# Kernel optimization log

Measured on AMD Instinct MI355X. Metric: run time of the kernel, lower is better.

The kernel has to match this reference:

```python
import jax, jax.numpy as jnp
import numpy as np

G = 128  # voxel grid extent per axis (positions are integer voxel coords in [0, G))
K = 3    # kernel size per axis -> 27 offsets


def setup_inputs() -> dict:
    key = jax.random.key(0)
    k1, k2, k3 = jax.random.split(key, 3)
    N, Cin, Cout = 500000, 32, 32
    features = jax.random.normal(k1, (N, Cin), dtype=jnp.float32)
    in_positions = jax.random.randint(k2, (N, 3), 0, G, dtype=jnp.int32)
    # learned conv weight: one [Cin, Cout] matrix per kernel offset (27 total)
    weight = jax.random.normal(k3, (K ** 3, Cin, Cout), dtype=jnp.float32) * 0.05
    return {"features": features, "in_positions": in_positions, "weight": weight}


def _hash(pos):
    # unique linear key for integer voxel coords in [0, G)^3
    return (pos[:, 0] * G + pos[:, 1]) * G + pos[:, 2]


def reference(features, in_positions, weight):
    # Submanifold sparse conv (kernel 3x3x3, odd -> offset 0, out_positions == in_positions,
    # voxel_size = 1.0, no bias, no normalize):
    # for each active voxel, gather active neighbors at each of the 27 kernel offsets,
    # transform with the per-offset weight matrix, and accumulate.
    N = features.shape[0]
    # dense hash table: voxel key -> row index in features, -1 if inactive
    table = jnp.full((G * G * G,), -1, dtype=jnp.int32)
    table = table.at[_hash(in_positions)].set(jnp.arange(N, dtype=jnp.int32))

    out = jnp.zeros((N, weight.shape[-1]), dtype=features.dtype)
    r = K // 2
    k = 0
    for dx in range(-r, r + 1):
        for dy in range(-r, r + 1):
            for dz in range(-r, r + 1):
                npos = in_positions + jnp.array([dx, dy, dz], dtype=jnp.int32)
                inside = jnp.all((npos >= 0) & (npos < G), axis=1)
                idx = table[jnp.where(inside, _hash(npos), 0)]
                valid = inside & (idx >= 0)
                # gather active neighbor features; zero where neighbor inactive
                gathered = jnp.where(valid[:, None], features[jnp.maximum(idx, 0)], 0.0)
                out = out + gathered @ weight[k]  # [N, Cout]
                k += 1
    return out
```

## Files before the change

kernel.cpp:

```cpp
#include <hip/hip_runtime.h>


#define GRID 128
#define CIN 32
#define COUT 32
#define NOFF 27

typedef __attribute__((ext_vector_type(8))) short bf16x8;
typedef __attribute__((ext_vector_type(4))) float f32x4;

__device__ inline unsigned short f2bf(float x) {
    union { float f; unsigned u; } v; v.f = x;
    unsigned r = v.u + 0x7fff + ((v.u >> 16) & 1);
    return (unsigned short)(r >> 16);
}

__global__ void prep_kernel(const float* __restrict__ feats,
                            const int* __restrict__ pos,
                            const float* __restrict__ wt,
                            int* __restrict__ table,
                            unsigned* __restrict__ featsB,
                            unsigned short* __restrict__ wtT,
                            int N, int elems4) {
    int i = blockIdx.x * 256 + threadIdx.x;
    if (i < elems4) {
        float4 v = *(const float4*)(feats + 4 * (size_t)i);
        unsigned lo = (unsigned)f2bf(v.x) | ((unsigned)f2bf(v.y) << 16);
        unsigned hi = (unsigned)f2bf(v.z) | ((unsigned)f2bf(v.w) << 16);
        uint2 o; o.x = lo; o.y = hi;
        *(uint2*)(featsB + 2 * (size_t)i) = o;
    }
    if (i < N) {
        int x = pos[3 * i], y = pos[3 * i + 1], z = pos[3 * i + 2];
        atomicMax(&table[(x * GRID + y) * GRID + z], i);
    }
    if (i < NOFF * CIN * COUT) {
        int k = i >> 10, r = i & 1023, ci = r >> 5, co = r & 31;
        wtT[k * 1024 + co * 32 + ci] = f2bf(wt[i]);
    }
}

__global__ __launch_bounds__(1024, 8)
void conv_kernel(const unsigned short* __restrict__ featsB,
                 const int* __restrict__ pos,
                 const unsigned short* __restrict__ wtT,
                 const int* __restrict__ table,
                 float* __restrict__ out, int N) {
    __shared__ __align__(16) unsigned short ldsw[NOFF * 1024];

    int tid = threadIdx.x;
    int wave = tid >> 6, lane = tid & 63;
    int m = lane & 15, quad = lane >> 4;
    int tile = blockIdx.x * 16 + wave;
    int base = tile * 16;
    int g = base + m;
    bool gv = g < N;

    int x = 0, y = 0, z = 0;
    if (gv) { x = pos[3 * g]; y = pos[3 * g + 1]; z = pos[3 * g + 2]; }
    int h = (x * GRID + y) * GRID + z;
    bool v0[3] = {gv && x > 0, gv, gv && x < GRID - 1};
    bool v1[3] = {gv && y > 0, gv, gv && y < GRID - 1};
    bool v2[3] = {gv && z > 0, gv, gv && z < GRID - 1};

    int ids[NOFF];
#pragma unroll
    for (int k = 0; k < NOFF; ++k) {
        const int dx = k / 9, dy = (k / 3) % 3, dz = k % 3;
        bool ok = v0[dx] && v1[dy] && v2[dz];
        int hk = h + (dx - 1) * GRID * GRID + (dy - 1) * GRID + (dz - 1);
        hk = ok ? hk : 0;
        int id = table[hk];
        ids[k] = ok ? id : -1;
    }

    {
        const uint4* src = (const uint4*)wtT;
        uint4* dst = (uint4*)ldsw;
        for (int e = tid; e < NOFF * 1024 * 2 / 16; e += 1024)
            dst[e] = src[e];
    }
    __syncthreads();

    f32x4 acc0 = {0.f, 0.f, 0.f, 0.f};
    f32x4 acc1 = {0.f, 0.f, 0.f, 0.f};
    const unsigned short* wb = ldsw + m * 32 + quad * 8;

#pragma unroll
    for (int k = 0; k < NOFF; ++k) {
        int id = ids[k];
        int row = (id >= 0 ? id : 0) * CIN;
        bf16x8 a = *(const bf16x8*)(featsB + row + quad * 8);
        if (id < 0) a = (bf16x8){0, 0, 0, 0, 0, 0, 0, 0};

        bf16x8 b0 = *(const bf16x8*)(wb + k * 1024);
        bf16x8 b1 = *(const bf16x8*)(wb + k * 1024 + 512);

        acc0 = __builtin_amdgcn_mfma_f32_16x16x32_bf16(a, b0, acc0, 0, 0, 0);
        acc1 = __builtin_amdgcn_mfma_f32_16x16x32_bf16(a, b1, acc1, 0, 0, 0);
    }

#pragma unroll
    for (int i = 0; i < 4; ++i) {
        int p = base + quad * 4 + i;
        if (p < N) {
            out[(size_t)p * COUT + m]      = acc0[i];
            out[(size_t)p * COUT + m + 16] = acc1[i];
        }
    }
}

extern "C" void kernel_launch(void* const* d_in, const int* in_sizes, int n_in,
                              void* d_out, int out_size, void* d_ws, size_t ws_size,
                              hipStream_t stream) {
    const float* feats = (const float*)d_in[0];
    const int*   pos   = (const int*)d_in[1];
    const float* wt    = (const float*)d_in[2];
    float* out = (float*)d_out;
    int N = in_sizes[0] / CIN;

    char* ws = (char*)d_ws;
    int* table = (int*)ws;
    size_t table_bytes = (size_t)GRID * GRID * GRID * sizeof(int);
    unsigned short* wtT = (unsigned short*)(ws + table_bytes);
    unsigned short* featsB = (unsigned short*)(ws + table_bytes + 65536);

    hipMemsetAsync(table, 0xFF, table_bytes, stream);

    int elems4 = N * CIN / 4;
    prep_kernel<<<(elems4 + 255) / 256, 256, 0, stream>>>(
        feats, pos, wt, table, (unsigned*)featsB, wtT, N, elems4);

    int numTiles = (N + 15) / 16;
    int blocks = (numTiles + 15) / 16;
    conv_kernel<<<blocks, 1024, 0, stream>>>(featsB, pos, wtT, table, out, N);
}
```

Baseline: 254.7 us.

## Sort voxels by Morton bucket to localize neighbor gathers, remap XCD blocks

Adds a counting sort of voxels into 32768 Morton-ordered 4x4x4 buckets (histogram, single-block scan, scatter). The hash table and bf16 features are rewritten in sorted order, and outputs are scattered back through origId. The aim is spatial locality, so neighbor feature gathers hit L2 cache. Block IDs are also remapped so contiguous tiles land on the same XCD, and weights are held in registers instead of being reread from LDS. In exchange it adds several kernels, a serial single-block scan, atomics and an indirect output scatter.

```diff
diff --git a/kernel.cpp b/kernel.cpp
--- a/kernel.cpp
+++ b/kernel.cpp
@@ -5,6 +5,7 @@
 #define CIN 32
 #define COUT 32
 #define NOFF 27
+#define NBUCKET 32768
 
 typedef __attribute__((ext_vector_type(8))) short bf16x8;
 typedef __attribute__((ext_vector_type(4))) float f32x4;
@@ -15,24 +16,29 @@
     return (unsigned short)(r >> 16);
 }
 
-__global__ void prep_kernel(const float* __restrict__ feats,
-                            const int* __restrict__ pos,
+__device__ inline unsigned spread3(unsigned v) {
+    v &= 31u;
+    v = (v | (v << 16)) & 0x030000FFu;
+    v = (v | (v << 8))  & 0x0300F00Fu;
+    v = (v | (v << 4))  & 0x030C30C3u;
+    v = (v | (v << 2))  & 0x09249249u;
+    return v;
+}
+__device__ inline int morton_bucket(int x, int y, int z) {
+    return (int)(spread3(x >> 2) | (spread3(y >> 2) << 1) | (spread3(z >> 2) << 2));
+}
+
+__global__ void hist_kernel(const int* __restrict__ pos,
                             const float* __restrict__ wt,
                             int* __restrict__ table,
-                            unsigned* __restrict__ featsB,
-                            unsigned short* __restrict__ wtT,
-                            int N, int elems4) {
+                            int* __restrict__ hist,
+                            unsigned short* __restrict__ wtT, int N) {
     int i = blockIdx.x * 256 + threadIdx.x;
-    if (i < elems4) {
-        float4 v = *(const float4*)(feats + 4 * (size_t)i);
-        unsigned lo = (unsigned)f2bf(v.x) | ((unsigned)f2bf(v.y) << 16);
-        unsigned hi = (unsigned)f2bf(v.z) | ((unsigned)f2bf(v.w) << 16);
-        uint2 o; o.x = lo; o.y = hi;
-        *(uint2*)(featsB + 2 * (size_t)i) = o;
-    }
     if (i < N) {
         int x = pos[3 * i], y = pos[3 * i + 1], z = pos[3 * i + 2];
-        atomicMax(&table[(x * GRID + y) * GRID + z], i);
+        int h = (x * GRID + y) * GRID + z;
+        atomicMax(&table[h], i);
+        atomicAdd(&hist[morton_bucket(x, y, z)], 1);
     }
     if (i < NOFF * CIN * COUT) {
         int k = i >> 10, r = i & 1023, ci = r >> 5, co = r & 31;
@@ -40,25 +46,86 @@
     }
 }
 
+__global__ __launch_bounds__(1024) void scan_kernel(int* __restrict__ hist) {
+    __shared__ int sums[1024];
+    int t = threadIdx.x;
+    int base = t * 32;
+    int v[32];
+#pragma unroll
+    for (int j = 0; j < 32; ++j) v[j] = hist[base + j];
+    int s = 0;
+#pragma unroll
+    for (int j = 0; j < 32; ++j) { int tmp = v[j]; v[j] = s; s += tmp; }
+    sums[t] = s;
+    __syncthreads();
+    for (int off = 1; off < 1024; off <<= 1) {
+        int add = (t >= off) ? sums[t - off] : 0;
+        __syncthreads();
+        sums[t] += add;
+        __syncthreads();
+    }
+    int excl = sums[t] - s;
+#pragma unroll
+    for (int j = 0; j < 32; ++j) hist[base + j] = excl + v[j];
+}
+
+__global__ void scatter_kernel(const int* __restrict__ pos,
+                               int* __restrict__ hist,
+                               int* __restrict__ table,
+                               int* __restrict__ keyS,
+                               int* __restrict__ origId, int N) {
+    int i = blockIdx.x * 256 + threadIdx.x;
+    if (i >= N) return;
+    int x = pos[3 * i], y = pos[3 * i + 1], z = pos[3 * i + 2];
+    int h = (x * GRID + y) * GRID + z;
+    int slot = atomicAdd(&hist[morton_bucket(x, y, z)], 1);
+    keyS[slot] = h;
+    origId[slot] = i;
+    if (table[h] == i) table[h] = -(slot + 2);
+}
+
+__global__ void convert_kernel(const float* __restrict__ feats,
+                               const int* __restrict__ origId,
+                               uint4* __restrict__ featsB, int N4) {
+    int j = blockIdx.x * 256 + threadIdx.x;
+    if (j >= N4) return;
+    int slot = j >> 2, t = j & 3;
+    int o = origId[slot];
+    const float4* s = (const float4*)(feats + (size_t)o * CIN + t * 8);
+    float4 a = s[0], b = s[1];
+    uint4 r;
+    r.x = (unsigned)f2bf(a.x) | ((unsigned)f2bf(a.y) << 16);
+    r.y = (unsigned)f2bf(a.z) | ((unsigned)f2bf(a.w) << 16);
+    r.z = (unsigned)f2bf(b.x) | ((unsigned)f2bf(b.y) << 16);
+    r.w = (unsigned)f2bf(b.z) | ((unsigned)f2bf(b.w) << 16);
+    featsB[j] = r;
+}
+
 __global__ __launch_bounds__(1024, 8)
 void conv_kernel(const unsigned short* __restrict__ featsB,
-                 const int* __restrict__ pos,
+                 const int* __restrict__ keyS,
                  const unsigned short* __restrict__ wtT,
                  const int* __restrict__ table,
+                 const int* __restrict__ origId,
                  float* __restrict__ out, int N) {
     __shared__ __align__(16) unsigned short ldsw[NOFF * 1024];
+
+    int nwg = (int)gridDim.x;
+    int orig = (int)blockIdx.x;
+    int q8 = nwg >> 3, r8 = nwg & 7;
+    int xcd = orig & 7, lin = orig >> 3;
+    int bid = (xcd < r8 ? xcd * (q8 + 1) : r8 * (q8 + 1) + (xcd - r8) * q8) + lin;
 
     int tid = threadIdx.x;
     int wave = tid >> 6, lane = tid & 63;
     int m = lane & 15, quad = lane >> 4;
-    int tile = blockIdx.x * 16 + wave;
+    int tile = bid * 16 + wave;
     int base = tile * 16;
     int g = base + m;
     bool gv = g < N;
 
-    int x = 0, y = 0, z = 0;
-    if (gv) { x = pos[3 * g]; y = pos[3 * g + 1]; z = pos[3 * g + 2]; }
-    int h = (x * GRID + y) * GRID + z;
+    int key = gv ? keyS[g] : 0;
+    int x = key >> 14, y = (key >> 7) & 127, z = key & 127;
     bool v0[3] = {gv && x > 0, gv, gv && x < GRID - 1};
     bool v1[3] = {gv && y > 0, gv, gv && y < GRID - 1};
     bool v2[3] = {gv && z > 0, gv, gv && z < GRID - 1};
@@ -68,7 +135,7 @@
     for (int k = 0; k < NOFF; ++k) {
         const int dx = k / 9, dy = (k / 3) % 3, dz = k % 3;
         bool ok = v0[dx] && v1[dy] && v2[dz];
-        int hk = h + (dx - 1) * GRID * GRID + (dy - 1) * GRID + (dz - 1);
+        int hk = key + (dx - 1) * GRID * GRID + (dy - 1) * GRID + (dz - 1);
         hk = ok ? hk : 0;
         int id = table[hk];
         ids[k] = ok ? id : -1;
@@ -77,35 +144,39 @@
     {
         const uint4* src = (const uint4*)wtT;
         uint4* dst = (uint4*)ldsw;
-        for (int e = tid; e < NOFF * 1024 * 2 / 16; e += 1024)
-            dst[e] = src[e];
+        for (int e = tid; e < NOFF * 1024 * 2 / 16; e += 1024) dst[e] = src[e];
     }
     __syncthreads();
+
+    bf16x8 w0[NOFF], w1[NOFF];
+    const unsigned short* wb = ldsw + m * 32 + quad * 8;
+#pragma unroll
+    for (int k = 0; k < NOFF; ++k) {
+        w0[k] = *(const bf16x8*)(wb + k * 1024);
+        w1[k] = *(const bf16x8*)(wb + k * 1024 + 512);
+    }
 
     f32x4 acc0 = {0.f, 0.f, 0.f, 0.f};
     f32x4 acc1 = {0.f, 0.f, 0.f, 0.f};
-    const unsigned short* wb = ldsw + m * 32 + quad * 8;
 
 #pragma unroll
     for (int k = 0; k < NOFF; ++k) {
         int id = ids[k];
-        int row = (id >= 0 ? id : 0) * CIN;
+        bool val = id < -1;
+        int row = val ? (-id - 2) * CIN : 0;
         bf16x8 a = *(const bf16x8*)(featsB + row + quad * 8);
-        if (id < 0) a = (bf16x8){0, 0, 0, 0, 0, 0, 0, 0};
-
-        bf16x8 b0 = *(const bf16x8*)(wb + k * 1024);
-        bf16x8 b1 = *(const bf16x8*)(wb + k * 1024 + 512);
-
-        acc0 = __builtin_amdgcn_mfma_f32_16x16x32_bf16(a, b0, acc0, 0, 0, 0);
-        acc1 = __builtin_amdgcn_mfma_f32_16x16x32_bf16(a, b1, acc1, 0, 0, 0);
+        if (!val) a = (bf16x8){0, 0, 0, 0, 0, 0, 0, 0};
+        acc0 = __builtin_amdgcn_mfma_f32_16x16x32_bf16(a, w0[k], acc0, 0, 0, 0);
+        acc1 = __builtin_amdgcn_mfma_f32_16x16x32_bf16(a, w1[k], acc1, 0, 0, 0);
     }
 
 #pragma unroll
     for (int i = 0; i < 4; ++i) {
         int p = base + quad * 4 + i;
         if (p < N) {
-            out[(size_t)p * COUT + m]      = acc0[i];
-            out[(size_t)p * COUT + m + 16] = acc1[i];
+            int o = origId[p];
+            out[(size_t)o * COUT + m]      = acc0[i];
+            out[(size_t)o * COUT + m + 16] = acc1[i];
         }
     }
 }
@@ -120,18 +191,25 @@
     int N = in_sizes[0] / CIN;
 
     char* ws = (char*)d_ws;
-    int* table = (int*)ws;
-    size_t table_bytes = (size_t)GRID * GRID * GRID * sizeof(int);
-    unsigned short* wtT = (unsigned short*)(ws + table_bytes);
-    unsigned short* featsB = (unsigned short*)(ws + table_bytes + 65536);
-
-    hipMemsetAsync(table, 0xFF, table_bytes, stream);
-
-    int elems4 = N * CIN / 4;
-    prep_kernel<<<(elems4 + 255) / 256, 256, 0, stream>>>(
-        feats, pos, wt, table, (unsigned*)featsB, wtT, N, elems4);
+    size_t off = 0;
+    int* table = (int*)(ws + off);            off += (size_t)GRID * GRID * GRID * 4;
+    unsigned short* wtT = (unsigned short*)(ws + off); off += 65536;
+    int* hist = (int*)(ws + off);             off += NBUCKET * 4;
+    int* keyS = (int*)(ws + off);             off += 2097152;
+    int* origId = (int*)(ws + off);           off += 2097152;
+    unsigned short* featsB = (unsigned short*)(ws + off);
+
+    hipMemsetAsync(table, 0xFF, (size_t)GRID * GRID * GRID * 4, stream);
+    hipMemsetAsync(hist, 0, NBUCKET * 4, stream);
+
+    int blocksN = (N + 255) / 256;
+    hist_kernel<<<blocksN, 256, 0, stream>>>(pos, wt, table, hist, wtT, N);
+    scan_kernel<<<1, 1024, 0, stream>>>(hist);
+    scatter_kernel<<<blocksN, 256, 0, stream>>>(pos, hist, table, keyS, origId, N);
+    convert_kernel<<<(N * 4 + 255) / 256, 256, 0, stream>>>(feats, origId,
+                                                            (uint4*)featsB, N * 4);
 
     int numTiles = (N + 15) / 16;
-    int blocks = (numTiles + 15) / 16;
-    conv_kernel<<<blocks, 1024, 0, stream>>>(featsB, pos, wtT, table, out, N);
-}
+    int nwg = (numTiles + 15) / 16;
+    conv_kernel<<<nwg, 1024, 0, stream>>>(featsB, keyS, wtT, table, origId, out, N);
+}
```

Result: slower. 314.5 us (+23.5%).

## Software-pipeline neighbor gathers with inline asm loads and a zero sentinel row

Applied to the files above, without the earlier changes.

Adds a zero row at the front of the bf16 feature buffer so missing neighbors point at it, which removes the per-offset masking. The 26 non-center gathers are issued through inline asm global loads in a six-deep rotating register pipeline with explicit vmcnt waits, overlapping gather latency with MFMA work. The center offset is computed from global memory before the LDS weight copy, so only 26 offsets are staged in LDS. Weights are also relaid out so the per-lane LDS reads are contiguous, and the workgroup shrinks to 512 threads. Hand-written waits and sched barriers constrain the compiler, and any mismatch in the vmcnt counts would read stale data.

```diff
diff --git a/kernel.cpp b/kernel.cpp
--- a/kernel.cpp
+++ b/kernel.cpp
@@ -19,86 +19,134 @@
                             const int* __restrict__ pos,
                             const float* __restrict__ wt,
                             int* __restrict__ table,
+                            unsigned short* __restrict__ wtT,
                             unsigned* __restrict__ featsB,
-                            unsigned short* __restrict__ wtT,
                             int N, int elems4) {
     int i = blockIdx.x * 256 + threadIdx.x;
     if (i < elems4) {
-        float4 v = *(const float4*)(feats + 4 * (size_t)i);
-        unsigned lo = (unsigned)f2bf(v.x) | ((unsigned)f2bf(v.y) << 16);
-        unsigned hi = (unsigned)f2bf(v.z) | ((unsigned)f2bf(v.w) << 16);
-        uint2 o; o.x = lo; o.y = hi;
-        *(uint2*)(featsB + 2 * (size_t)i) = o;
+        float4 v = ((const float4*)feats)[i];
+        uint2 o;
+        o.x = (unsigned)f2bf(v.x) | ((unsigned)f2bf(v.y) << 16);
+        o.y = (unsigned)f2bf(v.z) | ((unsigned)f2bf(v.w) << 16);
+        ((uint2*)featsB)[i + 8] = o;
     }
+    if (i < 8) ((uint2*)featsB)[i] = (uint2){0u, 0u};
     if (i < N) {
         int x = pos[3 * i], y = pos[3 * i + 1], z = pos[3 * i + 2];
         atomicMax(&table[(x * GRID + y) * GRID + z], i);
     }
     if (i < NOFF * CIN * COUT) {
         int k = i >> 10, r = i & 1023, ci = r >> 5, co = r & 31;
-        wtT[k * 1024 + co * 32 + ci] = f2bf(wt[i]);
+        int d = k * 1024 + (co >= 16 ? 512 : 0) + (ci >> 3) * 128 + (co & 15) * 8 + (ci & 7);
+        wtT[d] = f2bf(wt[i]);
     }
 }
 
-__global__ __launch_bounds__(1024, 8)
+#define SBAR() __builtin_amdgcn_sched_barrier(0)
+#define WAITV(n) asm volatile("s_waitcnt vmcnt(" #n ")" ::: "memory")
+#define GLOAD(dst, ss) \
+    asm volatile("global_load_dwordx4 %0, %1, %2" \
+                 : "=v"(dst) : "v"(voff[ss]), "s"(featsB));
+
+#define STEPL(areg, kk) { \
+    bf16x8 b0_ = *(const bf16x8*)(wb + (kk) * 1024); \
+    bf16x8 b1_ = *(const bf16x8*)(wb + (kk) * 1024 + 512); \
+    acc0 = __builtin_amdgcn_mfma_f32_16x16x32_bf16(areg, b0_, acc0, 0, 0, 0); \
+    acc1 = __builtin_amdgcn_mfma_f32_16x16x32_bf16(areg, b1_, acc1, 0, 0, 0); }
+
+__global__ __launch_bounds__(512, 6)
 void conv_kernel(const unsigned short* __restrict__ featsB,
                  const int* __restrict__ pos,
                  const unsigned short* __restrict__ wtT,
                  const int* __restrict__ table,
                  float* __restrict__ out, int N) {
-    __shared__ __align__(16) unsigned short ldsw[NOFF * 1024];
+    __shared__ __align__(16) unsigned short ldsw[26 * 1024];
 
     int tid = threadIdx.x;
     int wave = tid >> 6, lane = tid & 63;
     int m = lane & 15, quad = lane >> 4;
-    int tile = blockIdx.x * 16 + wave;
+    int tile = (int)blockIdx.x * 8 + wave;
     int base = tile * 16;
     int g = base + m;
     bool gv = g < N;
 
     int x = 0, y = 0, z = 0;
     if (gv) { x = pos[3 * g]; y = pos[3 * g + 1]; z = pos[3 * g + 2]; }
-    int h = (x * GRID + y) * GRID + z;
+    int key = (x * GRID + y) * GRID + z;
     bool v0[3] = {gv && x > 0, gv, gv && x < GRID - 1};
     bool v1[3] = {gv && y > 0, gv, gv && y < GRID - 1};
     bool v2[3] = {gv && z > 0, gv, gv && z < GRID - 1};
 
-    int ids[NOFF];
+    int qb = quad * 16;
+    int voff[26];
 #pragma unroll
-    for (int k = 0; k < NOFF; ++k) {
+    for (int s = 0; s < 26; ++s) {
+        const int k = s + (s >= 13);
         const int dx = k / 9, dy = (k / 3) % 3, dz = k % 3;
         bool ok = v0[dx] && v1[dy] && v2[dz];
-        int hk = h + (dx - 1) * GRID * GRID + (dy - 1) * GRID + (dz - 1);
+        int hk = key + (dx - 1) * GRID * GRID + (dy - 1) * GRID + (dz - 1);
         hk = ok ? hk : 0;
         int id = table[hk];
-        ids[k] = ok ? id : -1;
+        voff[s] = ((ok && id >= 0) ? (id + 1) * 64 : 0) + qb;
     }
+
+    f32x4 acc0 = {0.f, 0.f, 0.f, 0.f};
+    f32x4 acc1 = {0.f, 0.f, 0.f, 0.f};
+
+    {
+        int idc = table[key];
+        int vc = ((gv && idc >= 0) ? (idc + 1) * 64 : 0) + qb;
+        bf16x8 ac = *(const bf16x8*)((const char*)featsB + vc);
+        const unsigned short* wc = wtT + 13 * 1024 + quad * 128 + m * 8;
+        bf16x8 wc0 = *(const bf16x8*)(wc);
+        bf16x8 wc1 = *(const bf16x8*)(wc + 512);
+        acc0 = __builtin_amdgcn_mfma_f32_16x16x32_bf16(ac, wc0, acc0, 0, 0, 0);
+        acc1 = __builtin_amdgcn_mfma_f32_16x16x32_bf16(ac, wc1, acc1, 0, 0, 0);
+    }
+    SBAR();
+
+    bf16x8 c0, c1, c2, c3, c4, c5;
+    GLOAD(c0, 0) GLOAD(c1, 1) GLOAD(c2, 2)
+    GLOAD(c3, 3) GLOAD(c4, 4) GLOAD(c5, 5)
 
     {
         const uint4* src = (const uint4*)wtT;
         uint4* dst = (uint4*)ldsw;
-        for (int e = tid; e < NOFF * 1024 * 2 / 16; e += 1024)
-            dst[e] = src[e];
+        for (int e = tid; e < 26 * 128; e += 512) {
+            int ks = e >> 7; ks += (ks >= 13);
+            dst[e] = src[ks * 128 + (e & 127)];
+        }
     }
     __syncthreads();
 
-    f32x4 acc0 = {0.f, 0.f, 0.f, 0.f};
-    f32x4 acc1 = {0.f, 0.f, 0.f, 0.f};
-    const unsigned short* wb = ldsw + m * 32 + quad * 8;
+    const unsigned short* wb = ldsw + quad * 128 + m * 8;
 
-#pragma unroll
-    for (int k = 0; k < NOFF; ++k) {
-        int id = ids[k];
-        int row = (id >= 0 ? id : 0) * CIN;
-        bf16x8 a = *(const bf16x8*)(featsB + row + quad * 8);
-        if (id < 0) a = (bf16x8){0, 0, 0, 0, 0, 0, 0, 0};
-
-        bf16x8 b0 = *(const bf16x8*)(wb + k * 1024);
-        bf16x8 b1 = *(const bf16x8*)(wb + k * 1024 + 512);
-
-        acc0 = __builtin_amdgcn_mfma_f32_16x16x32_bf16(a, b0, acc0, 0, 0, 0);
-        acc1 = __builtin_amdgcn_mfma_f32_16x16x32_bf16(a, b1, acc1, 0, 0, 0);
-    }
+    WAITV(5); SBAR(); STEPL(c0, 0)  GLOAD(c0, 6)
+    WAITV(5); SBAR(); STEPL(c1, 1)  GLOAD(c1, 7)
+    WAITV(5); SBAR(); STEPL(c2, 2)  GLOAD(c2, 8)
+    WAITV(5); SBAR(); STEPL(c3, 3)  GLOAD(c3, 9)
+    WAITV(5); SBAR(); STEPL(c4, 4)  GLOAD(c4, 10)
+    WAITV(5); SBAR(); STEPL(c5, 5)  GLOAD(c5, 11)
+    WAITV(5); SBAR(); STEPL(c0, 6)  GLOAD(c0, 12)
+    WAITV(5); SBAR(); STEPL(c1, 7)  GLOAD(c1, 13)
+    WAITV(5); SBAR(); STEPL(c2, 8)  GLOAD(c2, 14)
+    WAITV(5); SBAR(); STEPL(c3, 9)  GLOAD(c3, 15)
+    WAITV(5); SBAR(); STEPL(c4, 10) GLOAD(c4, 16)
+    WAITV(5); SBAR(); STEPL(c5, 11) GLOAD(c5, 17)
+    WAITV(5); SBAR(); STEPL(c0, 12) GLOAD(c0, 18)
+    WAITV(5); SBAR(); STEPL(c1, 13) GLOAD(c1, 19)
+    WAITV(5); SBAR(); STEPL(c2, 14) GLOAD(c2, 20)
+    WAITV(5); SBAR(); STEPL(c3, 15) GLOAD(c3, 21)
+    WAITV(5); SBAR(); STEPL(c4, 16) GLOAD(c4, 22)
+    WAITV(5); SBAR(); STEPL(c5, 17) GLOAD(c5, 23)
+    WAITV(5); SBAR(); STEPL(c0, 18) GLOAD(c0, 24)
+    WAITV(5); SBAR(); STEPL(c1, 19) GLOAD(c1, 25)
+    WAITV(5); SBAR(); STEPL(c2, 20)
+    WAITV(4); SBAR(); STEPL(c3, 21)
+    WAITV(3); SBAR(); STEPL(c4, 22)
+    WAITV(2); SBAR(); STEPL(c5, 23)
+    WAITV(1); SBAR(); STEPL(c0, 24)
+    WAITV(0); SBAR(); STEPL(c1, 25)
 
 #pragma unroll
     for (int i = 0; i < 4; ++i) {
@@ -120,18 +168,19 @@
     int N = in_sizes[0] / CIN;
 
     char* ws = (char*)d_ws;
-    int* table = (int*)ws;
-    size_t table_bytes = (size_t)GRID * GRID * GRID * sizeof(int);
-    unsigned short* wtT = (unsigned short*)(ws + table_bytes);
-    unsigned short* featsB = (unsigned short*)(ws + table_bytes + 65536);
+    size_t off = 0;
+    int* table = (int*)(ws + off);            off += (size_t)GRID * GRID * GRID * 4;
+    unsigned short* wtT = (unsigned short*)(ws + off); off += 65536;
+    unsigned* featsB = (unsigned*)(ws + off);
 
-    hipMemsetAsync(table, 0xFF, table_bytes, stream);
+    hipMemsetAsync(table, 0xFF, (size_t)GRID * GRID * GRID * 4, stream);
 
     int elems4 = N * CIN / 4;
     prep_kernel<<<(elems4 + 255) / 256, 256, 0, stream>>>(
-        feats, pos, wt, table, (unsigned*)featsB, wtT, N, elems4);
+        feats, pos, wt, table, wtT, featsB, N, elems4);
 
     int numTiles = (N + 15) / 16;
-    int blocks = (numTiles + 15) / 16;
-    conv_kernel<<<blocks, 1024, 0, stream>>>(featsB, pos, wtT, table, out, N);
+    int nwg = (numTiles + 7) / 8;
+    conv_kernel<<<nwg, 512, 0, stream>>>((const unsigned short*)featsB, pos, wtT,
+                                         table, out, N);
 }
```

Result: no change. 255.9 us (+0.5%).
